# Kernel optimization log

Hardware: AMD Instinct MI355X
Metric: run time of the kernel (lower is better)

Reference implementation:

```python
import jax, jax.numpy as jnp
import numpy as np

NUM_LABELS = 128
START_LABEL = 126
STOP_LABEL = 127
B, T = 128, 2048


def setup_inputs() -> dict:
    key = jax.random.key(0)
    k1, k2 = jax.random.split(key)
    emissions = jax.random.normal(k1, (B, T, NUM_LABELS), dtype=jnp.float32)
    transitions = jax.random.normal(k2, (NUM_LABELS, NUM_LABELS), dtype=jnp.float32)
    # __init__ zeroing: no transition INTO start, none OUT of stop
    transitions = transitions.at[:, START_LABEL].set(0.0)
    transitions = transitions.at[STOP_LABEL, :].set(0.0)
    return {"emissions": emissions, "transitions": transitions}


def reference(emissions, transitions):
    # Viterbi max-sum recurrence, faithful to the torch decode():
    #   v_0 = -10000 everywhere except start label (=0); emissions[:, 0] is NOT added.
    #   v_i[b, j] = max_k (v_{i-1}[b, k] + transitions[k, j]) + emissions[b, i, j]
    #   final: v += transitions[:, stop]; take max over labels.
    b, t, L = emissions.shape
    v0 = jnp.full((b, L), -10000.0, dtype=emissions.dtype).at[:, START_LABEL].set(0.0)

    def step(v, e_t):
        # scores: [B, L_from, L_to]
        scores = v[:, :, None] + transitions[None, :, :]
        v_new = jnp.max(scores, axis=1) + e_t
        return v_new, None

    # time-major emissions for steps 1..T-1
    em_t = jnp.swapaxes(emissions, 0, 1)[1:]  # [T-1, B, L]
    v, _ = jax.lax.scan(step, v0, em_t)
    v = v + transitions[:, STOP_LABEL][None, :]
    best_final_score = jnp.max(v, axis=-1)      # [B]
    best_final_label = jnp.argmax(v, axis=-1)   # [B]
    return best_final_score, best_final_label
```

## Files before the change

### kernel.cpp

```cpp
#include <hip/hip_runtime.h>

#define NB 128
#define NT 2048
#define NL 128
#define START_LBL 126
#define STOP_LBL 127

typedef float f4 __attribute__((ext_vector_type(4)));

__device__ __forceinline__ float bcast_lane(float v, int l) {
    return __int_as_float(__builtin_amdgcn_readlane(__float_as_int(v), l));
}

__global__ __launch_bounds__(512, 2) void crf_viterbi(
    const float* __restrict__ em, const float* __restrict__ tr,
    float* __restrict__ out)
{
    const int b    = blockIdx.x;
    const int tid  = threadIdx.x;
    const int w    = tid >> 6;
    const int lane = tid & 63;
    const int j0   = lane;
    const int j1   = lane + 64;
    const int kbase = w << 4;
    const int l15  = lane & 15;
    const int jj   = kbase + l15;

    __shared__ __align__(16) float part[2][NL][12];
    __shared__ __align__(16) float elds[2][32][NL];
    __shared__ float vfin[NL];

    float trA[16], trB[16];
#pragma unroll
    for (int kk = 0; kk < 16; ++kk) {
        trA[kk] = tr[(kbase + kk) * NL + j0];
        trB[kk] = tr[(kbase + kk) * NL + j1];
    }

    const float* eb = em + (size_t)b * NT * NL;

    {
        const float* src = eb + tid * 4;
        float* dst = &elds[0][0][0] + tid * 4;
        __builtin_amdgcn_global_load_lds(
            (const __attribute__((address_space(1))) void*)src,
            (__attribute__((address_space(3))) void*)dst, 16, 0, 0);
        __builtin_amdgcn_global_load_lds(
            (const __attribute__((address_space(1))) void*)(src + 2048),
            (__attribute__((address_space(3))) void*)(dst + 2048), 16, 0, 0);
    }
    __syncthreads();

    float vv = (jj == START_LBL) ? 0.0f : -10000.0f;

    const int col = (w + (lane >> 3)) & 7;

#pragma unroll 2
    for (int t = 1; t < NT; ++t) {
        const int pb = t & 1;

        float e = elds[(t >> 5) & 1][t & 31][jj];

        if ((t & 31) == 1 && t < NT - 32) {
            const int tcn = (t >> 5) + 1;
            const float* src = eb + (size_t)tcn * 32 * NL + tid * 4;
            float* dst = &elds[tcn & 1][0][0] + tid * 4;
            __builtin_amdgcn_global_load_lds(
                (const __attribute__((address_space(1))) void*)src,
                (__attribute__((address_space(3))) void*)dst, 16, 0, 0);
            __builtin_amdgcn_global_load_lds(
                (const __attribute__((address_space(1))) void*)(src + 2048),
                (__attribute__((address_space(3))) void*)(dst + 2048), 16, 0, 0);
        }

        float vb[16];
#pragma unroll
        for (int kk = 0; kk < 16; ++kk) vb[kk] = bcast_lane(vv, kk);

        float a0 = fmaxf(vb[0] + trA[0], vb[1] + trA[1]);
        float a1 = fmaxf(vb[0] + trB[0], vb[1] + trB[1]);
#pragma unroll
        for (int kk = 2; kk < 16; kk += 2) {
            float x0 = vb[kk]     + trA[kk];
            float x1 = vb[kk + 1] + trA[kk + 1];
            a0 = fmaxf(fmaxf(a0, x0), x1);
            float y0 = vb[kk]     + trB[kk];
            float y1 = vb[kk + 1] + trB[kk + 1];
            a1 = fmaxf(fmaxf(a1, y0), y1);
        }

        part[pb][j0][col] = a0;
        part[pb][j1][col] = a1;

        if ((t & 31) == 31) {
            __syncthreads();
        } else {
            asm volatile("s_waitcnt lgkmcnt(0)\n\ts_barrier" ::: "memory");
        }

        f4 pa = *(const f4*)&part[pb][jj][0];
        f4 pc = *(const f4*)&part[pb][jj][4];
        float m = fmaxf(fmaxf(pa.x, pa.y), pa.z);
        m = fmaxf(fmaxf(m, pa.w), pc.x);
        m = fmaxf(fmaxf(m, pc.y), pc.z);
        m = fmaxf(m, pc.w);
        vv = m + e;
    }

    float vf = vv + tr[jj * NL + STOP_LBL];
    if (lane < 16) vfin[jj] = vf;
    __syncthreads();

    if (tid < 64) {
        float v0 = vfin[tid];
        float v1 = vfin[tid + 64];
        float val; int idx;
        if (v1 > v0) { val = v1; idx = tid + 64; } else { val = v0; idx = tid; }
#pragma unroll
        for (int off = 32; off >= 1; off >>= 1) {
            float ov = __shfl_xor(val, off, 64);
            int   oi = __shfl_xor(idx, off, 64);
            if (ov > val || (ov == val && oi < idx)) { val = ov; idx = oi; }
        }
        if (tid == 0) {
            out[b]      = val;
            out[NB + b] = (float)idx;
        }
    }
}

extern "C" void kernel_launch(void* const* d_in, const int* in_sizes, int n_in,
                              void* d_out, int out_size, void* d_ws, size_t ws_size,
                              hipStream_t stream) {
    const float* em = (const float*)d_in[0];
    const float* tr = (const float*)d_in[1];
    float* out = (float*)d_out;
    crf_viterbi<<<NB, 512, 0, stream>>>(em, tr, out);
}
```

Measured before the change: 914.7 us.

## Use 4 waves per batch with 32-row k-slices and packed f2 add

Cuts the per-batch block from 8 to 4 waves, so each wave covers 32 source labels instead of 16 and the cross-wave partial-max reduction reads 4 partials instead of 8. The inner add is written on float2 vectors so the compiler can emit packed adds, and two accumulator chains shorten the max dependency chain. The aim is to make the per-step barrier and LDS exchange cheaper, since fewer waves take part. The cost is twice the serial per-wave work per timestep (32 readlanes and adds) and more registers for transitions.

```diff
diff --git a/kernel.cpp b/kernel.cpp
--- a/kernel.cpp
+++ b/kernel.cpp
@@ -7,12 +7,13 @@
 #define STOP_LBL 127
 
 typedef float f4 __attribute__((ext_vector_type(4)));
+typedef float f2 __attribute__((ext_vector_type(2)));
 
 __device__ __forceinline__ float bcast_lane(float v, int l) {
     return __int_as_float(__builtin_amdgcn_readlane(__float_as_int(v), l));
 }
 
-__global__ __launch_bounds__(512, 2) void crf_viterbi(
+__global__ __launch_bounds__(256, 1) void crf_viterbi(
     const float* __restrict__ em, const float* __restrict__ tr,
     float* __restrict__ out)
 {
@@ -22,38 +23,36 @@
     const int lane = tid & 63;
     const int j0   = lane;
     const int j1   = lane + 64;
-    const int kbase = w << 4;
-    const int l15  = lane & 15;
-    const int jj   = kbase + l15;
+    const int kbase = w << 5;
+    const int l31  = lane & 31;
+    const int jj   = kbase + l31;
 
-    __shared__ __align__(16) float part[2][NL][12];
+    __shared__ __align__(16) float part[2][NL][4];
     __shared__ __align__(16) float elds[2][32][NL];
     __shared__ float vfin[NL];
 
-    float trA[16], trB[16];
+    f2 t2[32];
 #pragma unroll
-    for (int kk = 0; kk < 16; ++kk) {
-        trA[kk] = tr[(kbase + kk) * NL + j0];
-        trB[kk] = tr[(kbase + kk) * NL + j1];
+    for (int kk = 0; kk < 32; ++kk) {
+        t2[kk].x = tr[(kbase + kk) * NL + j0];
+        t2[kk].y = tr[(kbase + kk) * NL + j1];
     }
 
     const float* eb = em + (size_t)b * NT * NL;
 
-    {
-        const float* src = eb + tid * 4;
-        float* dst = &elds[0][0][0] + tid * 4;
+#pragma unroll
+    for (int i = 0; i < 4; ++i) {
+        const float* src = eb + i * 1024 + tid * 4;
+        float* dst = &elds[0][0][0] + i * 1024 + tid * 4;
         __builtin_amdgcn_global_load_lds(
             (const __attribute__((address_space(1))) void*)src,
             (__attribute__((address_space(3))) void*)dst, 16, 0, 0);
-        __builtin_amdgcn_global_load_lds(
-            (const __attribute__((address_space(1))) void*)(src + 2048),
-            (__attribute__((address_space(3))) void*)(dst + 2048), 16, 0, 0);
     }
     __syncthreads();
 
     float vv = (jj == START_LBL) ? 0.0f : -10000.0f;
 
-    const int col = (w + (lane >> 3)) & 7;
+    const int col = (w + (lane >> 4)) & 3;
 
 #pragma unroll 2
     for (int t = 1; t < NT; ++t) {
@@ -63,31 +62,42 @@
 
         if ((t & 31) == 1 && t < NT - 32) {
             const int tcn = (t >> 5) + 1;
-            const float* src = eb + (size_t)tcn * 32 * NL + tid * 4;
-            float* dst = &elds[tcn & 1][0][0] + tid * 4;
-            __builtin_amdgcn_global_load_lds(
-                (const __attribute__((address_space(1))) void*)src,
-                (__attribute__((address_space(3))) void*)dst, 16, 0, 0);
-            __builtin_amdgcn_global_load_lds(
-                (const __attribute__((address_space(1))) void*)(src + 2048),
-                (__attribute__((address_space(3))) void*)(dst + 2048), 16, 0, 0);
+            const float* srcb = eb + (size_t)tcn * 32 * NL;
+            float* dstb = &elds[tcn & 1][0][0];
+#pragma unroll
+            for (int i = 0; i < 4; ++i) {
+                __builtin_amdgcn_global_load_lds(
+                    (const __attribute__((address_space(1))) void*)(srcb + i * 1024 + tid * 4),
+                    (__attribute__((address_space(3))) void*)(dstb + i * 1024 + tid * 4),
+                    16, 0, 0);
+            }
         }
 
-        float vb[16];
+        float a0A = -3.0e38f, a0B = -3.0e38f;
+        float a1A = -3.0e38f, a1B = -3.0e38f;
 #pragma unroll
-        for (int kk = 0; kk < 16; ++kk) vb[kk] = bcast_lane(vv, kk);
-
-        float a0 = fmaxf(vb[0] + trA[0], vb[1] + trA[1]);
-        float a1 = fmaxf(vb[0] + trB[0], vb[1] + trB[1]);
+        for (int half = 0; half < 2; ++half) {
+            float s[16];
 #pragma unroll
-        for (int kk = 2; kk < 16; kk += 2) {
-            float x0 = vb[kk]     + trA[kk];
-            float x1 = vb[kk + 1] + trA[kk + 1];
-            a0 = fmaxf(fmaxf(a0, x0), x1);
-            float y0 = vb[kk]     + trB[kk];
-            float y1 = vb[kk + 1] + trB[kk + 1];
-            a1 = fmaxf(fmaxf(a1, y0), y1);
+            for (int kk = 0; kk < 16; ++kk)
+                s[kk] = bcast_lane(vv, half * 16 + kk);
+#pragma unroll
+            for (int kk = 0; kk < 16; kk += 2) {
+                f2 sv0; sv0.x = s[kk];     sv0.y = s[kk];
+                f2 sv1; sv1.x = s[kk + 1]; sv1.y = s[kk + 1];
+                f2 r0 = t2[half * 16 + kk]     + sv0;
+                f2 r1 = t2[half * 16 + kk + 1] + sv1;
+                if ((kk & 2) == 0) {
+                    a0A = fmaxf(fmaxf(a0A, r0.x), r1.x);
+                    a1A = fmaxf(fmaxf(a1A, r0.y), r1.y);
+                } else {
+                    a0B = fmaxf(fmaxf(a0B, r0.x), r1.x);
+                    a1B = fmaxf(fmaxf(a1B, r0.y), r1.y);
+                }
+            }
         }
+        float a0 = fmaxf(a0A, a0B);
+        float a1 = fmaxf(a1A, a1B);
 
         part[pb][j0][col] = a0;
         part[pb][j1][col] = a1;
@@ -99,16 +109,12 @@
         }
 
         f4 pa = *(const f4*)&part[pb][jj][0];
-        f4 pc = *(const f4*)&part[pb][jj][4];
-        float m = fmaxf(fmaxf(pa.x, pa.y), pa.z);
-        m = fmaxf(fmaxf(m, pa.w), pc.x);
-        m = fmaxf(fmaxf(m, pc.y), pc.z);
-        m = fmaxf(m, pc.w);
+        float m = fmaxf(fmaxf(pa.x, pa.y), fmaxf(pa.z, pa.w));
         vv = m + e;
     }
 
     float vf = vv + tr[jj * NL + STOP_LBL];
-    if (lane < 16) vfin[jj] = vf;
+    if (lane < 32) vfin[jj] = vf;
     __syncthreads();
 
     if (tid < 64) {
@@ -135,5 +141,5 @@
     const float* em = (const float*)d_in[0];
     const float* tr = (const float*)d_in[1];
     float* out = (float*)d_out;
-    crf_viterbi<<<NB, 512, 0, stream>>>(em, tr, out);
+    crf_viterbi<<<NB, 256, 0, stream>>>(em, tr, out);
 }
```

Measured after the change: 832.8 us. -9.0%, faster.
